# Kernel optimization log

Measured on AMD Instinct MI355X. Metric: run time of the kernel, lower is better.

## Reference

```python
import jax, jax.numpy as jnp
import numpy as np
import math

SQRT2 = math.sqrt(2.0)
SQRT_2PI = math.sqrt(2.0 * math.pi)
T = 1.0


def _margin_from_bn(xt_flat):
    # xt_flat: [B, C*L]. torch .std() is unbiased (ddof=1).
    std = jnp.abs(jnp.std(xt_flat, axis=1, ddof=1))  # [B]
    mean = jnp.mean(xt_flat, axis=1)                  # [B]
    z = -mean / std
    cdf = 0.5 * (1.0 + jax.lax.erf(z / SQRT2))        # norm.cdf(-mean/std)
    safe_cdf = jnp.maximum(cdf, 1e-30)                # guard div; branch selected by where
    margin_a = -std * jnp.exp(-(mean / std) ** 2 / 2.0) / SQRT_2PI / safe_cdf + mean
    margin = jnp.where(cdf > 0.001, margin_a, -3.0 * std)
    # original detaches margin (computed on CPU via numpy/scipy)
    return jax.lax.stop_gradient(margin)


def reference(x_s, x_t, x_ts, x_st, i):
    B, C = x_ts.shape[0], x_ts.shape[1]
    xs = x_ts.reshape(B, C, -1)  # source: [B, C, L]
    xt = x_st.reshape(B, C, -1)  # target: [B, C, L]
    margin = _margin_from_bn(xt.reshape(B, -1))  # [B]
    # distillation_loss(source=xs, target=xt, T, dims=1, margin)
    target = jnp.maximum(xt / T, margin[:, None, None])
    entropy = jax.nn.softmax(xs / T, axis=1) * jax.nn.log_softmax(target / T, axis=1)
    channel_entropy = -jnp.sum(entropy, axis=1)          # [B, L]
    batch_mean_entropy = jnp.mean(channel_entropy, axis=1)  # [B]
    loss = jnp.mean(batch_mean_entropy)
    return (loss, entropy)


def setup_inputs() -> dict:
    key = jax.random.key(0)
    k1, k2, k3, k4 = jax.random.split(key, 4)
    return {
        "x_s": jax.random.normal(k1, (1,), dtype=jnp.float32),
        "x_t": jax.random.normal(k2, (1,), dtype=jnp.float32),
        "x_ts": jax.random.normal(k3, (8, 1024, 64, 64), dtype=jnp.float32),
        "x_st": jax.random.normal(k4, (8, 1024, 64, 64), dtype=jnp.float32),
        "i": 0,
    }
```

## Files before the change

### kernel.cpp

```cpp
#include <hip/hip_runtime.h>
#include <math.h>

#define BB 8
#define CC 1024
#define LL 4096
#define NPB (CC*LL)
#define TOTAL (BB*CC*LL)


__global__ void k_batch_sums(const float* __restrict__ xt, double* __restrict__ sums) {
    int b = blockIdx.y;
    const float4* p = (const float4*)(xt + (size_t)b * NPB);
    int t = blockIdx.x * blockDim.x + threadIdx.x;
    double s1 = 0.0, s2 = 0.0;
    #pragma unroll
    for (int j4 = 0; j4 < 4; ++j4) {
        float4 v[4];
        #pragma unroll
        for (int k = 0; k < 4; ++k) v[k] = p[(size_t)(j4 * 4 + k) * 65536 + t];
        #pragma unroll
        for (int k = 0; k < 4; ++k) {
            float q1 = (v[k].x + v[k].y) + (v[k].z + v[k].w);
            float q2 = (v[k].x * v[k].x + v[k].y * v[k].y)
                     + (v[k].z * v[k].z + v[k].w * v[k].w);
            s1 += (double)q1;
            s2 += (double)q2;
        }
    }
    for (int off = 32; off; off >>= 1) {
        s1 += __shfl_down(s1, off, 64);
        s2 += __shfl_down(s2, off, 64);
    }
    __shared__ double ls1[4], ls2[4];
    int lane = threadIdx.x & 63, w = threadIdx.x >> 6;
    if (lane == 0) { ls1[w] = s1; ls2[w] = s2; }
    __syncthreads();
    if (threadIdx.x == 0) {
        atomicAdd(&sums[2 * b],     ls1[0] + ls1[1] + ls1[2] + ls1[3]);
        atomicAdd(&sums[2 * b + 1], ls2[0] + ls2[1] + ls2[2] + ls2[3]);
    }
}

__global__ void k_margin(const double* __restrict__ sums, float* __restrict__ margin) {
    int b = threadIdx.x;
    if (b < BB) {
        double n = (double)NPB;
        double s1 = sums[2 * b], s2 = sums[2 * b + 1];
        double mean = s1 / n;
        double var = (s2 - s1 * s1 / n) / (n - 1.0);
        double sd = sqrt(var);
        double z = -mean / sd;
        double cdf = 0.5 * (1.0 + erf(z / 1.4142135623730951));
        double safe = fmax(cdf, 1e-30);
        double r = mean / sd;
        double ma = -sd * exp(-r * r * 0.5) / 2.5066282746310002 / safe + mean;
        double m = (cdf > 0.001) ? ma : -3.0 * sd;
        margin[b] = (float)m;
    }
}

__global__ void k_colstats(const float* __restrict__ xs, const float* __restrict__ xt,
                           const float* __restrict__ margin,
                           float* __restrict__ ssA, float* __restrict__ syA) {
    int lane = threadIdx.x & 63, w = threadIdx.x >> 6;
    int l0 = blockIdx.x * 256 + lane * 4;
    int b = blockIdx.y;
    int c0 = blockIdx.z * 64 + w;
    float mg = margin[b];
    const float* ps = xs + (size_t)b * NPB + l0;
    const float* pt = xt + (size_t)b * NPB + l0;
    float ss[4] = {0, 0, 0, 0}, sy[4] = {0, 0, 0, 0};
    #pragma unroll
    for (int j4 = 0; j4 < 4; ++j4) {
        float4 vs[4], vt[4];
        #pragma unroll
        for (int k = 0; k < 4; ++k) {
            int c = c0 + 4 * (j4 * 4 + k);
            vs[k] = *(const float4*)(ps + (size_t)c * LL);
            vt[k] = *(const float4*)(pt + (size_t)c * LL);
        }
        #pragma unroll
        for (int k = 0; k < 4; ++k) {
            ss[0] += __expf(vs[k].x); ss[1] += __expf(vs[k].y);
            ss[2] += __expf(vs[k].z); ss[3] += __expf(vs[k].w);
            sy[0] += __expf(fmaxf(vt[k].x, mg)); sy[1] += __expf(fmaxf(vt[k].y, mg));
            sy[2] += __expf(fmaxf(vt[k].z, mg)); sy[3] += __expf(fmaxf(vt[k].w, mg));
        }
    }
    __shared__ float red[4][64][8];
    #pragma unroll
    for (int k = 0; k < 4; ++k) { red[w][lane][k] = ss[k]; red[w][lane][4 + k] = sy[k]; }
    __syncthreads();
    if (w == 0) {
        #pragma unroll
        for (int k = 0; k < 4; ++k) {
            float vss = red[0][lane][k] + red[1][lane][k] + red[2][lane][k] + red[3][lane][k];
            float vsy = red[0][lane][4+k] + red[1][lane][4+k] + red[2][lane][4+k] + red[3][lane][4+k];
            atomicAdd(&ssA[b * LL + l0 + k], vss);
            atomicAdd(&syA[b * LL + l0 + k], vsy);
        }
    }
}

__global__ void k_entropy(const float* __restrict__ xs, const float* __restrict__ xt,
                          const float* __restrict__ margin,
                          const float* __restrict__ ssA, const float* __restrict__ syA,
                          float* __restrict__ out1, double* __restrict__ lossAcc) {
    int lane = threadIdx.x & 63, w = threadIdx.x >> 6;
    int l0 = blockIdx.x * 256 + lane * 4;
    int b = blockIdx.y;
    int c0 = blockIdx.z * 64 + w;
    float mg = margin[b];
    float4 ssv = *(const float4*)(ssA + b * LL + l0);
    float4 syv = *(const float4*)(syA + b * LL + l0);
    float A0 = __logf(ssv.x), A1 = __logf(ssv.y), A2 = __logf(ssv.z), A3 = __logf(ssv.w);
    float B0 = __logf(syv.x), B1 = __logf(syv.y), B2 = __logf(syv.z), B3 = __logf(syv.w);
    const float* ps = xs + (size_t)b * NPB + l0;
    const float* pt = xt + (size_t)b * NPB + l0;
    float* po = out1 + (size_t)b * NPB + l0;
    float acc = 0.f;
    #pragma unroll
    for (int j4 = 0; j4 < 4; ++j4) {
        float4 vs[4], vt[4];
        int cbase = c0 + 4 * (j4 * 4);
        #pragma unroll
        for (int k = 0; k < 4; ++k) {
            int c = cbase + 4 * k;
            vs[k] = *(const float4*)(ps + (size_t)c * LL);
            vt[k] = *(const float4*)(pt + (size_t)c * LL);
        }
        #pragma unroll
        for (int k = 0; k < 4; ++k) {
            int c = cbase + 4 * k;
            float4 e;
            e.x = __expf(vs[k].x - A0) * (fmaxf(vt[k].x, mg) - B0);
            e.y = __expf(vs[k].y - A1) * (fmaxf(vt[k].y, mg) - B1);
            e.z = __expf(vs[k].z - A2) * (fmaxf(vt[k].z, mg) - B2);
            e.w = __expf(vs[k].w - A3) * (fmaxf(vt[k].w, mg) - B3);
            *(float4*)(po + (size_t)c * LL) = e;
            acc += (e.x + e.y) + (e.z + e.w);
        }
    }
    for (int off = 32; off; off >>= 1) acc += __shfl_down(acc, off, 64);
    __shared__ float wacc[4];
    if (lane == 0) wacc[w] = acc;
    __syncthreads();
    if (threadIdx.x == 0) {
        double t = (double)wacc[0] + wacc[1] + wacc[2] + wacc[3];
        atomicAdd(lossAcc, t);
    }
}

__global__ void k_finalize(const double* __restrict__ lossAcc, float* __restrict__ out) {
    if (threadIdx.x == 0) out[0] = (float)(-lossAcc[0] / (double)(BB * LL));
}

extern "C" void kernel_launch(void* const* d_in, const int* in_sizes, int n_in,
                              void* d_out, int out_size, void* d_ws, size_t ws_size,
                              hipStream_t stream) {
    const float* x_ts = (const float*)d_in[2];
    const float* x_st = (const float*)d_in[3];
    float* out = (float*)d_out;

    double* sums    = (double*)d_ws;
    double* lossAcc = (double*)((char*)d_ws + 128);
    float*  margins = (float*)((char*)d_ws + 192);
    float*  ssA     = (float*)((char*)d_ws + 256);
    float*  syA     = (float*)((char*)d_ws + 256 + 131072);

    hipMemsetAsync(d_ws, 0, 256 + 262144, stream);

    k_batch_sums<<<dim3(256, BB), 256, 0, stream>>>(x_st, sums);
    k_margin<<<1, 64, 0, stream>>>(sums, margins);
    k_colstats<<<dim3(16, BB, 16), 256, 0, stream>>>(x_ts, x_st, margins, ssA, syA);
    k_entropy<<<dim3(16, BB, 16), 256, 0, stream>>>(x_ts, x_st, margins, ssA, syA,
                                                    out + 1, lossAcc);
    k_finalize<<<1, 64, 0, stream>>>(lossAcc, out);
}
```

Baseline: 388.1 us.

## Fuse all stages into one cooperative persistent kernel with grid syncs

Replaces the five separate kernels (batch sums, margin, column stats, entropy, finalize) with a single cooperative kernel of 512 blocks that uses grid-wide syncs between phases. Each block now covers 256 channels instead of 64, and the margin is computed per block in shared memory. The goal is to remove launch overhead and inter-kernel gaps. In exchange there are three grid barriers, far fewer blocks (two per CU by launch bounds), and possibly less latency hiding, on a workload dominated by memory bandwidth from reading about 256MB twice and writing 128MB.

After: 564.6 us. 45.5% more time.

```diff
diff --git a/kernel.cpp b/kernel.cpp
--- a/kernel.cpp
+++ b/kernel.cpp
@@ -1,5 +1,8 @@
 #include <hip/hip_runtime.h>
+#include <hip/hip_cooperative_groups.h>
 #include <math.h>
+
+namespace cg = cooperative_groups;
 
 #define BB 8
 #define CC 1024
@@ -8,42 +11,46 @@
 #define TOTAL (BB*CC*LL)
 
 
-__global__ void k_batch_sums(const float* __restrict__ xt, double* __restrict__ sums) {
-    int b = blockIdx.y;
-    const float4* p = (const float4*)(xt + (size_t)b * NPB);
-    int t = blockIdx.x * blockDim.x + threadIdx.x;
-    double s1 = 0.0, s2 = 0.0;
-    #pragma unroll
-    for (int j4 = 0; j4 < 4; ++j4) {
-        float4 v[4];
-        #pragma unroll
-        for (int k = 0; k < 4; ++k) v[k] = p[(size_t)(j4 * 4 + k) * 65536 + t];
-        #pragma unroll
-        for (int k = 0; k < 4; ++k) {
-            float q1 = (v[k].x + v[k].y) + (v[k].z + v[k].w);
-            float q2 = (v[k].x * v[k].x + v[k].y * v[k].y)
-                     + (v[k].z * v[k].z + v[k].w * v[k].w);
+__global__ __launch_bounds__(256, 2)
+void k_fused(const float* __restrict__ xs, const float* __restrict__ xt,
+             double* __restrict__ sums, double* __restrict__ lossAcc,
+             float* __restrict__ ssA, float* __restrict__ syA,
+             float* __restrict__ out) {
+    cg::grid_group grid = cg::this_grid();
+    const int tid = threadIdx.x;
+    const int lane = tid & 63, w = tid >> 6;
+    const int bx = blockIdx.x, b = blockIdx.y, bz = blockIdx.z;
+
+    __shared__ float red[4][64][8];
+    __shared__ double ls[8];
+    __shared__ float shMargin;
+
+    {
+        const float4* p = (const float4*)(xt + (size_t)b * NPB);
+        int t = (bx * 4 + bz) * 256 + tid;
+        double s1 = 0.0, s2 = 0.0;
+        #pragma unroll 4
+        for (int i = 0; i < 64; ++i) {
+            float4 v = p[t + (size_t)i * 16384];
+            float q1 = (v.x + v.y) + (v.z + v.w);
+            float q2 = (v.x * v.x + v.y * v.y) + (v.z * v.z + v.w * v.w);
             s1 += (double)q1;
             s2 += (double)q2;
         }
+        for (int off = 32; off; off >>= 1) {
+            s1 += __shfl_down(s1, off, 64);
+            s2 += __shfl_down(s2, off, 64);
+        }
+        if (lane == 0) { ls[w] = s1; ls[4 + w] = s2; }
+        __syncthreads();
+        if (tid == 0) {
+            atomicAdd(&sums[2 * b],     ls[0] + ls[1] + ls[2] + ls[3]);
+            atomicAdd(&sums[2 * b + 1], ls[4] + ls[5] + ls[6] + ls[7]);
+        }
     }
-    for (int off = 32; off; off >>= 1) {
-        s1 += __shfl_down(s1, off, 64);
-        s2 += __shfl_down(s2, off, 64);
-    }
-    __shared__ double ls1[4], ls2[4];
-    int lane = threadIdx.x & 63, w = threadIdx.x >> 6;
-    if (lane == 0) { ls1[w] = s1; ls2[w] = s2; }
-    __syncthreads();
-    if (threadIdx.x == 0) {
-        atomicAdd(&sums[2 * b],     ls1[0] + ls1[1] + ls1[2] + ls1[3]);
-        atomicAdd(&sums[2 * b + 1], ls2[0] + ls2[1] + ls2[2] + ls2[3]);
-    }
-}
+    grid.sync();
 
-__global__ void k_margin(const double* __restrict__ sums, float* __restrict__ margin) {
-    int b = threadIdx.x;
-    if (b < BB) {
+    if (tid == 0) {
         double n = (double)NPB;
         double s1 = sums[2 * b], s2 = sums[2 * b + 1];
         double mean = s1 / n;
@@ -54,105 +61,92 @@
         double safe = fmax(cdf, 1e-30);
         double r = mean / sd;
         double ma = -sd * exp(-r * r * 0.5) / 2.5066282746310002 / safe + mean;
-        double m = (cdf > 0.001) ? ma : -3.0 * sd;
-        margin[b] = (float)m;
+        shMargin = (float)((cdf > 0.001) ? ma : -3.0 * sd);
     }
-}
+    __syncthreads();
+    const float mg = shMargin;
 
-__global__ void k_colstats(const float* __restrict__ xs, const float* __restrict__ xt,
-                           const float* __restrict__ margin,
-                           float* __restrict__ ssA, float* __restrict__ syA) {
-    int lane = threadIdx.x & 63, w = threadIdx.x >> 6;
-    int l0 = blockIdx.x * 256 + lane * 4;
-    int b = blockIdx.y;
-    int c0 = blockIdx.z * 64 + w;
-    float mg = margin[b];
+    const int l0 = bx * 256 + lane * 4;
+    const int c0 = (bz * 4 + w) * 64;
     const float* ps = xs + (size_t)b * NPB + l0;
     const float* pt = xt + (size_t)b * NPB + l0;
-    float ss[4] = {0, 0, 0, 0}, sy[4] = {0, 0, 0, 0};
-    #pragma unroll
-    for (int j4 = 0; j4 < 4; ++j4) {
-        float4 vs[4], vt[4];
+    {
+        float ss[4] = {0, 0, 0, 0}, sy[4] = {0, 0, 0, 0};
+        #pragma unroll 2
+        for (int j = 0; j < 16; ++j) {
+            float4 vs[4], vt[4];
+            #pragma unroll
+            for (int k = 0; k < 4; ++k) {
+                int c = c0 + j * 4 + k;
+                vs[k] = *(const float4*)(ps + (size_t)c * LL);
+                vt[k] = *(const float4*)(pt + (size_t)c * LL);
+            }
+            #pragma unroll
+            for (int k = 0; k < 4; ++k) {
+                ss[0] += __expf(vs[k].x); ss[1] += __expf(vs[k].y);
+                ss[2] += __expf(vs[k].z); ss[3] += __expf(vs[k].w);
+                sy[0] += __expf(fmaxf(vt[k].x, mg)); sy[1] += __expf(fmaxf(vt[k].y, mg));
+                sy[2] += __expf(fmaxf(vt[k].z, mg)); sy[3] += __expf(fmaxf(vt[k].w, mg));
+            }
+        }
+        __syncthreads();
         #pragma unroll
-        for (int k = 0; k < 4; ++k) {
-            int c = c0 + 4 * (j4 * 4 + k);
-            vs[k] = *(const float4*)(ps + (size_t)c * LL);
-            vt[k] = *(const float4*)(pt + (size_t)c * LL);
-        }
-        #pragma unroll
-        for (int k = 0; k < 4; ++k) {
-            ss[0] += __expf(vs[k].x); ss[1] += __expf(vs[k].y);
-            ss[2] += __expf(vs[k].z); ss[3] += __expf(vs[k].w);
-            sy[0] += __expf(fmaxf(vt[k].x, mg)); sy[1] += __expf(fmaxf(vt[k].y, mg));
-            sy[2] += __expf(fmaxf(vt[k].z, mg)); sy[3] += __expf(fmaxf(vt[k].w, mg));
+        for (int k = 0; k < 4; ++k) { red[w][lane][k] = ss[k]; red[w][lane][4 + k] = sy[k]; }
+        __syncthreads();
+        if (w == 0) {
+            #pragma unroll
+            for (int k = 0; k < 4; ++k) {
+                float vss = red[0][lane][k] + red[1][lane][k] + red[2][lane][k] + red[3][lane][k];
+                float vsy = red[0][lane][4+k] + red[1][lane][4+k] + red[2][lane][4+k] + red[3][lane][4+k];
+                atomicAdd(&ssA[b * LL + l0 + k], vss);
+                atomicAdd(&syA[b * LL + l0 + k], vsy);
+            }
         }
     }
-    __shared__ float red[4][64][8];
-    #pragma unroll
-    for (int k = 0; k < 4; ++k) { red[w][lane][k] = ss[k]; red[w][lane][4 + k] = sy[k]; }
-    __syncthreads();
-    if (w == 0) {
-        #pragma unroll
-        for (int k = 0; k < 4; ++k) {
-            float vss = red[0][lane][k] + red[1][lane][k] + red[2][lane][k] + red[3][lane][k];
-            float vsy = red[0][lane][4+k] + red[1][lane][4+k] + red[2][lane][4+k] + red[3][lane][4+k];
-            atomicAdd(&ssA[b * LL + l0 + k], vss);
-            atomicAdd(&syA[b * LL + l0 + k], vsy);
+    grid.sync();
+
+    {
+        float4 ssv = *(const float4*)(ssA + b * LL + l0);
+        float4 syv = *(const float4*)(syA + b * LL + l0);
+        float A0 = __logf(ssv.x), A1 = __logf(ssv.y), A2 = __logf(ssv.z), A3 = __logf(ssv.w);
+        float B0 = __logf(syv.x), B1 = __logf(syv.y), B2 = __logf(syv.z), B3 = __logf(syv.w);
+        float* po = out + 1 + (size_t)b * NPB + l0;
+        float acc = 0.f;
+        #pragma unroll 2
+        for (int j = 0; j < 16; ++j) {
+            float4 vs[4], vt[4];
+            #pragma unroll
+            for (int k = 0; k < 4; ++k) {
+                int c = c0 + j * 4 + k;
+                vs[k] = *(const float4*)(ps + (size_t)c * LL);
+                vt[k] = *(const float4*)(pt + (size_t)c * LL);
+            }
+            #pragma unroll
+            for (int k = 0; k < 4; ++k) {
+                int c = c0 + j * 4 + k;
+                float4 e;
+                e.x = __expf(vs[k].x - A0) * (fmaxf(vt[k].x, mg) - B0);
+                e.y = __expf(vs[k].y - A1) * (fmaxf(vt[k].y, mg) - B1);
+                e.z = __expf(vs[k].z - A2) * (fmaxf(vt[k].z, mg) - B2);
+                e.w = __expf(vs[k].w - A3) * (fmaxf(vt[k].w, mg) - B3);
+                *(float4*)(po + (size_t)c * LL) = e;
+                acc += (e.x + e.y) + (e.z + e.w);
+            }
+        }
+        for (int off = 32; off; off >>= 1) acc += __shfl_down(acc, off, 64);
+        __syncthreads();
+        if (lane == 0) red[0][0][w + 4] = acc;
+        __syncthreads();
+        if (tid == 0) {
+            double t = (double)red[0][0][4] + red[0][0][5] + red[0][0][6] + red[0][0][7];
+            atomicAdd(lossAcc, t);
         }
     }
-}
+    grid.sync();
 
-__global__ void k_entropy(const float* __restrict__ xs, const float* __restrict__ xt,
-                          const float* __restrict__ margin,
-                          const float* __restrict__ ssA, const float* __restrict__ syA,
-                          float* __restrict__ out1, double* __restrict__ lossAcc) {
-    int lane = threadIdx.x & 63, w = threadIdx.x >> 6;
-    int l0 = blockIdx.x * 256 + lane * 4;
-    int b = blockIdx.y;
-    int c0 = blockIdx.z * 64 + w;
-    float mg = margin[b];
-    float4 ssv = *(const float4*)(ssA + b * LL + l0);
-    float4 syv = *(const float4*)(syA + b * LL + l0);
-    float A0 = __logf(ssv.x), A1 = __logf(ssv.y), A2 = __logf(ssv.z), A3 = __logf(ssv.w);
-    float B0 = __logf(syv.x), B1 = __logf(syv.y), B2 = __logf(syv.z), B3 = __logf(syv.w);
-    const float* ps = xs + (size_t)b * NPB + l0;
-    const float* pt = xt + (size_t)b * NPB + l0;
-    float* po = out1 + (size_t)b * NPB + l0;
-    float acc = 0.f;
-    #pragma unroll
-    for (int j4 = 0; j4 < 4; ++j4) {
-        float4 vs[4], vt[4];
-        int cbase = c0 + 4 * (j4 * 4);
-        #pragma unroll
-        for (int k = 0; k < 4; ++k) {
-            int c = cbase + 4 * k;
-            vs[k] = *(const float4*)(ps + (size_t)c * LL);
-            vt[k] = *(const float4*)(pt + (size_t)c * LL);
-        }
-        #pragma unroll
-        for (int k = 0; k < 4; ++k) {
-            int c = cbase + 4 * k;
-            float4 e;
-            e.x = __expf(vs[k].x - A0) * (fmaxf(vt[k].x, mg) - B0);
-            e.y = __expf(vs[k].y - A1) * (fmaxf(vt[k].y, mg) - B1);
-            e.z = __expf(vs[k].z - A2) * (fmaxf(vt[k].z, mg) - B2);
-            e.w = __expf(vs[k].w - A3) * (fmaxf(vt[k].w, mg) - B3);
-            *(float4*)(po + (size_t)c * LL) = e;
-            acc += (e.x + e.y) + (e.z + e.w);
-        }
+    if (bx == 0 && b == 0 && bz == 0 && tid == 0) {
+        out[0] = (float)(-lossAcc[0] / (double)(BB * LL));
     }
-    for (int off = 32; off; off >>= 1) acc += __shfl_down(acc, off, 64);
-    __shared__ float wacc[4];
-    if (lane == 0) wacc[w] = acc;
-    __syncthreads();
-    if (threadIdx.x == 0) {
-        double t = (double)wacc[0] + wacc[1] + wacc[2] + wacc[3];
-        atomicAdd(lossAcc, t);
-    }
-}
-
-__global__ void k_finalize(const double* __restrict__ lossAcc, float* __restrict__ out) {
-    if (threadIdx.x == 0) out[0] = (float)(-lossAcc[0] / (double)(BB * LL));
 }
 
 extern "C" void kernel_launch(void* const* d_in, const int* in_sizes, int n_in,
@@ -164,16 +158,13 @@
 
     double* sums    = (double*)d_ws;
     double* lossAcc = (double*)((char*)d_ws + 128);
-    float*  margins = (float*)((char*)d_ws + 192);
     float*  ssA     = (float*)((char*)d_ws + 256);
     float*  syA     = (float*)((char*)d_ws + 256 + 131072);
 
     hipMemsetAsync(d_ws, 0, 256 + 262144, stream);
 
-    k_batch_sums<<<dim3(256, BB), 256, 0, stream>>>(x_st, sums);
-    k_margin<<<1, 64, 0, stream>>>(sums, margins);
-    k_colstats<<<dim3(16, BB, 16), 256, 0, stream>>>(x_ts, x_st, margins, ssA, syA);
-    k_entropy<<<dim3(16, BB, 16), 256, 0, stream>>>(x_ts, x_st, margins, ssA, syA,
-                                                    out + 1, lossAcc);
-    k_finalize<<<1, 64, 0, stream>>>(lossAcc, out);
+    void* args[] = { (void*)&x_ts, (void*)&x_st, (void*)&sums, (void*)&lossAcc,
+                     (void*)&ssA, (void*)&syA, (void*)&out };
+    hipLaunchCooperativeKernel((void*)k_fused, dim3(16, BB, 4), dim3(256),
+                               args, 0, stream);
 }
```
